# Kernel optimization log

Hardware: AMD Instinct MI355X
Metric: run time of the kernel (lower is better)

## Reference

```python
import jax, jax.numpy as jnp
import numpy as np

HID = 64; H = 2; D = 32; L = 2; G = 64; F_IN = 771
NA = 120000; NE = 60000; E0 = 1500000; E1 = 1000000; E2 = 1000000


def _seg_mean(x, seg, n):
    s = jax.ops.segment_sum(x, seg, num_segments=n)
    c = jax.ops.segment_sum(jnp.ones((x.shape[0], 1), x.dtype), seg, num_segments=n)
    return s / jnp.maximum(c, 1.0)


def setup_inputs() -> dict:
    ks = jax.random.split(jax.random.key(0), 32)
    r = lambda i, s: 0.02 * jax.random.normal(ks[i], s, jnp.float32)
    z = lambda s: jnp.zeros(s, jnp.float32)
    inp = {}
    inp['x_argument'] = jax.random.normal(ks[0], (NA, F_IN), jnp.float32)
    inp['x_evidence'] = jax.random.normal(ks[1], (NE, F_IN), jnp.float32)
    inp['Win'] = r(2, (2, F_IN, HID)); inp['b_in'] = z((2, HID))
    inp['Wk'] = r(3, (L, 2, HID, HID)); inp['bk'] = z((L, 2, HID))
    inp['Wq'] = r(4, (L, 2, HID, HID)); inp['bq'] = z((L, 2, HID))
    inp['Wv'] = r(5, (L, 2, HID, HID)); inp['bv'] = z((L, 2, HID))
    inp['Wa'] = r(6, (L, 2, HID, HID)); inp['ba'] = z((L, 2, HID))
    inp['skip'] = jnp.ones((L, 2), jnp.float32)
    inp['Watt'] = r(7, (L, 3, H, D, D)); inp['Wmsg'] = r(8, (L, 3, H, D, D))
    inp['prel'] = jnp.ones((L, 3, H), jnp.float32)
    inp['Wnews'] = r(9, (384, HID)); inp['bnews'] = z((HID,))
    inp['Wdeb'] = r(10, (HID, HID)); inp['bdeb'] = z((HID,))
    inp['Wqm'] = r(11, (HID, HID)); inp['bqm'] = z((HID,))
    inp['Wkm'] = r(12, (HID, HID)); inp['bkm'] = z((HID,))
    inp['Wvm'] = r(13, (HID, HID)); inp['bvm'] = z((HID,))
    inp['Wom'] = r(14, (HID, HID)); inp['bom'] = z((HID,))
    inp['Wc1'] = r(15, (2 * HID, 64)); inp['bc1'] = z((64,))
    inp['Wc2'] = r(16, (64, 1)); inp['bc2'] = z((1,))
    inp['e0_src'] = jax.random.randint(ks[17], (E0,), 0, NA)
    inp['e0_dst'] = jax.random.randint(ks[18], (E0,), 0, NA)
    inp['e1_src'] = jax.random.randint(ks[19], (E1,), 0, NE)
    inp['e1_dst'] = jax.random.randint(ks[20], (E1,), 0, NA)
    inp['e2_src'] = jax.random.randint(ks[21], (E2,), 0, NA)
    inp['e2_dst'] = jax.random.randint(ks[22], (E2,), 0, NE)
    inp['batch_arg'] = jnp.sort(jax.random.randint(ks[23], (NA,), 0, G))
    return inp


def reference(x_argument, x_evidence, Win, b_in, Wk, bk, Wq, bq, Wv, bv, Wa, ba,
              skip, Watt, Wmsg, prel, Wnews, bnews, Wdeb, bdeb,
              Wqm, bqm, Wkm, bkm, Wvm, bvm, Wom, bom, Wc1, bc1, Wc2, bc2,
              e0_src, e0_dst, e1_src, e1_dst, e2_src, e2_dst, batch_arg):
    # Claim embedding from RAW features (slice 384:768), pooled per graph.
    claim_raw = _seg_mean(x_argument[:, 384:768], batch_arg, G)
    # Per-node-type input projection + ReLU. type 0 = argument, 1 = evidence.
    xs = [jax.nn.relu(x_argument @ Win[0] + b_in[0]),
          jax.nn.relu(x_evidence @ Win[1] + b_in[1])]
    # (src_type, dst_type, src_idx, dst_idx) for each heterogeneous edge type.
    edges = [(0, 0, e0_src, e0_dst), (1, 0, e1_src, e1_dst), (0, 1, e2_src, e2_dst)]
    scale = 1.0 / jnp.sqrt(jnp.float32(D))
    for l in range(L):  # HGTConv stack
        Kt = [(xs[t] @ Wk[l, t] + bk[l, t]).reshape(-1, H, D) for t in range(2)]
        Qt = [(xs[t] @ Wq[l, t] + bq[l, t]).reshape(-1, H, D) for t in range(2)]
        Vt = [(xs[t] @ Wv[l, t] + bv[l, t]).reshape(-1, H, D) for t in range(2)]
        buf = {0: [], 1: []}
        for e, (s, d, src, dst) in enumerate(edges):
            k2 = jnp.einsum('ehd,hdf->ehf', Kt[s][src], Watt[l, e])  # relation key transform
            v2 = jnp.einsum('ehd,hdf->ehf', Vt[s][src], Wmsg[l, e])  # relation msg transform
            sc = (Qt[d][dst] * k2).sum(-1) * prel[l, e] * scale      # (E, H)
            buf[d].append((sc, dst, v2))
        new_xs = []
        for d in range(2):
            n = xs[d].shape[0]
            sc = jnp.concatenate([b[0] for b in buf[d]], 0)
            dst = jnp.concatenate([b[1] for b in buf[d]], 0)
            v2 = jnp.concatenate([b[2] for b in buf[d]], 0)
            # segment softmax over all incoming edges of each destination node
            m = jax.ops.segment_max(sc, dst, num_segments=n)
            ex = jnp.exp(sc - m[dst])
            den = jax.ops.segment_sum(ex, dst, num_segments=n)
            alpha = ex / den[dst]
            agg = jax.ops.segment_sum(alpha[..., None] * v2, dst, num_segments=n).reshape(n, HID)
            out = jax.nn.gelu(agg, approximate=False) @ Wa[l, d] + ba[l, d]
            beta = jax.nn.sigmoid(skip[l, d])
            new_xs.append(beta * out + (1.0 - beta) * xs[d])
        xs = new_xs
    graph_emb = _seg_mean(xs[0], batch_arg, G)
    eF = claim_raw @ Wnews + bnews          # (G, HID)
    g = graph_emb @ Wdeb + bdeb             # (G, HID)
    # MultiheadAttention with query len 1 and key len 1: softmax over a single
    # key is identically 1, so attn_out == out_proj(v_proj(g)) exactly
    # (Wqm/bqm/Wkm/bkm receive exactly zero gradient, matching torch).
    v = g @ Wvm + bvm
    attn_out = v @ Wom + bom
    h = jax.nn.relu(jnp.concatenate([g, attn_out], -1) @ Wc1 + bc1)  # dropout is eval-mode identity
    return h @ Wc2 + bc2  # (G, 1)
```

## Files before the change

kernel.cpp:

```cpp
#include <hip/hip_runtime.h>
#include <math.h>

#define N0 120000
#define N1 60000
#define E0N 1500000
#define E1N 1000000
#define E2N 1000000
#define FIN 771
#define NG 64
#define KSTEPS_IN 25

#define GB0 ((N0 + 127) / 128)
#define GB1 ((N1 + 127) / 128)
#define AB0 ((N0 + 3) / 4)
#define AB1 ((N1 + 3) / 4)
#define SB0 ((N0 + 1023) / 1024)
#define SB1 ((N1 + 1023) / 1024)
#define PREPB 70

#define Q0O   ((size_t)0)
#define KV00O ((size_t)N0 * 64)
#define KV02O ((size_t)N0 * 192)
#define Q1O   ((size_t)N0 * 320)
#define KV11O ((size_t)N0 * 320 + (size_t)N1 * 64)

typedef __attribute__((ext_vector_type(8))) short short8;
typedef __attribute__((ext_vector_type(4))) float f32x4;
typedef __attribute__((ext_vector_type(4))) unsigned short ushort4v;
typedef unsigned short ushort;

__device__ __forceinline__ float gelu_f(float v) {
    return 0.5f * v * (1.f + erff(v * 0.70710678118654752f));
}
__device__ __forceinline__ ushort f2b(float f) {
    union { float f; unsigned u; } v; v.f = f;
    unsigned u = v.u;
    return (ushort)((u + 0x7FFFu + ((u >> 16) & 1u)) >> 16);
}
__device__ __forceinline__ float lo16(unsigned u) {
    union { unsigned x; float f; } v; v.x = u << 16; return v.f;
}
__device__ __forceinline__ float hi16(unsigned u) {
    union { unsigned x; float f; } v; v.x = u & 0xFFFF0000u; return v.f;
}
__device__ __forceinline__ int asi(float f) { union { float f; int i; } v; v.f = f; return v.i; }
__device__ __forceinline__ float asf(int i) { union { int i; float f; } v; v.i = i; return v.f; }

#define GLOAD_LDS16(gsrc, ldst) __builtin_amdgcn_global_load_lds( \
    (const __attribute__((address_space(1))) void*)(gsrc),        \
    (__attribute__((address_space(3))) void*)(ldst), 16, 0, 0)

__device__ __forceinline__ void proj_phase(
    const ushort* xls, int type, int l, int w, int lane, int r0, int nrows,
    const ushort* __restrict__ Wpack, const float* __restrict__ bpack,
    ushort* __restrict__ projAll)
{
    short8 bfr[2][2];
    #pragma unroll
    for (int ksp = 0; ksp < 2; ++ksp)
        #pragma unroll
        for (int rb = 0; rb < 2; ++rb)
            bfr[ksp][rb] = *(const short8*)&xls[(w * 32 + rb * 16 + (lane & 15)) * 72
                                                + ksp * 32 + (lane >> 4) * 8];
    const int nslots = type ? 3 : 5;
    const int sbase = l * 8 + (type ? 5 : 0);
    const int c0b = (lane >> 4) * 4;

    for (int slot = 0; slot < nslots; ++slot) {
        const ushort* Wp = Wpack + (size_t)(sbase + slot) * 4096;
        const float* bias = bpack + (size_t)(sbase + slot) * 64;
        size_t ooff; unsigned pitch, qs, ph;
        if (slot == 0) { ooff = type ? Q1O : Q0O; pitch = 64; qs = 4; ph = 0; }
        else {
            int kv = (slot + 1) >> 1;
            ooff = type ? KV11O : (kv == 1 ? KV00O : KV02O);
            pitch = 128; qs = 8; ph = (slot & 1) ? 0u : 4u;
        }
        ushort* out = projAll + ooff;
        f32x4 acc[2][4] = {};
        #pragma unroll
        for (int ksp = 0; ksp < 2; ++ksp) {
            const ushort* wb = Wp + ksp * 2048 + lane * 8;
            #pragma unroll
            for (int cg = 0; cg < 4; ++cg) {
                short8 afr = *(const short8*)&wb[cg * 512];
                acc[0][cg] = __builtin_amdgcn_mfma_f32_16x16x32_bf16(afr, bfr[ksp][0], acc[0][cg], 0, 0, 0);
                acc[1][cg] = __builtin_amdgcn_mfma_f32_16x16x32_bf16(afr, bfr[ksp][1], acc[1][cg], 0, 0, 0);
            }
        }
        #pragma unroll
        for (int rb = 0; rb < 2; ++rb) {
            int r = r0 + rb * 16 + (lane & 15);
            if (r < nrows) {
                #pragma unroll
                for (int cg = 0; cg < 4; ++cg) {
                    int c = cg * 16 + c0b;
                    ushort4v o;
                    o[0] = f2b(acc[rb][cg][0] + bias[c + 0]);
                    o[1] = f2b(acc[rb][cg][1] + bias[c + 1]);
                    o[2] = f2b(acc[rb][cg][2] + bias[c + 2]);
                    o[3] = f2b(acc[rb][cg][3] + bias[c + 3]);
                    *(ushort4v*)&out[(size_t)r * pitch + (unsigned)(c >> 2) * qs + ph] = o;
                }
            }
        }
    }
}

__global__ __launch_bounds__(256) void inproj_proj_kernel(
    const float* __restrict__ xa, const float* __restrict__ xe,
    const ushort* __restrict__ Wpin, const float* __restrict__ b_in,
    float* __restrict__ xs0, float* __restrict__ xs1,
    const ushort* __restrict__ Wpack, const float* __restrict__ bpack,
    ushort* __restrict__ projAll)
{
    __shared__ union {
        float stage[2][4096];
        ushort xls[128 * 72];
    } sm;
    const int bx = blockIdx.x;
    const int type = (bx >= GB0) ? 1 : 0;
    const float* __restrict__ x = type ? xe : xa;
    const int nrows = type ? N1 : N0;
    const ushort* __restrict__ Wp = Wpin + (type ? (size_t)KSTEPS_IN * 2048 : 0);
    const float* __restrict__ bias = b_in + type * 64;
    float* __restrict__ out = type ? xs1 : xs0;

    const int tid = threadIdx.x, w = tid >> 6, lane = tid & 63;
    const int r0b = (type ? bx - GB0 : bx) * 128;
    const int r0 = r0b + w * 32;
    const float* xlim = x + ((size_t)nrows * FIN - 4);

    const int srow = (lane >> 3);
    const int scol = (lane & 7) * 4;

    f32x4 acc[2][4] = {};

    #pragma unroll
    for (int i = 0; i < 4; ++i) {
        int inst = w * 4 + i;
        int grow = min(r0b + inst * 8 + srow, nrows - 1);
        const float* src = x + (size_t)grow * FIN + scol;
        if (src > xlim) src = xlim;
        GLOAD_LDS16(src, &sm.stage[0][inst * 256]);
    }
    __syncthreads();

    for (int ks = 0; ks < KSTEPS_IN; ++ks) {
        if (ks + 1 < KSTEPS_IN) {
            const int k0 = (ks + 1) * 32;
            float* dbuf = sm.stage[(ks + 1) & 1];
            #pragma unroll
            for (int i = 0; i < 4; ++i) {
                int inst = w * 4 + i;
                int grow = min(r0b + inst * 8 + srow, nrows - 1);
                const float* src = x + (size_t)grow * FIN + k0 + scol;
                if (src > xlim) src = xlim;
                GLOAD_LDS16(src, &dbuf[inst * 256]);
            }
        }
        const float* bufc = sm.stage[ks & 1];
        short8 bfr[2];
        #pragma unroll
        for (int rb = 0; rb < 2; ++rb) {
            int row = w * 32 + rb * 16 + (lane & 15);
            const float* p = bufc + row * 32 + (lane >> 4) * 8;
            float4 f0 = *(const float4*)p;
            float4 f1 = *(const float4*)(p + 4);
            short8 t;
            t[0] = (short)f2b(f0.x); t[1] = (short)f2b(f0.y);
            t[2] = (short)f2b(f0.z); t[3] = (short)f2b(f0.w);
            t[4] = (short)f2b(f1.x); t[5] = (short)f2b(f1.y);
            t[6] = (short)f2b(f1.z); t[7] = (short)f2b(f1.w);
            bfr[rb] = t;
        }
        const ushort* wb = Wp + (size_t)ks * 2048 + lane * 8;
        #pragma unroll
        for (int cg = 0; cg < 4; ++cg) {
            short8 afr = *(const short8*)&wb[cg * 512];
            acc[0][cg] = __builtin_amdgcn_mfma_f32_16x16x32_bf16(afr, bfr[0], acc[0][cg], 0, 0, 0);
            acc[1][cg] = __builtin_amdgcn_mfma_f32_16x16x32_bf16(afr, bfr[1], acc[1][cg], 0, 0, 0);
        }
        __syncthreads();
    }

    const int c0b = (lane >> 4) * 4;
    #pragma unroll
    for (int rb = 0; rb < 2; ++rb) {
        int lrow = w * 32 + rb * 16 + (lane & 15);
        int r = r0b + lrow;
        #pragma unroll
        for (int cg = 0; cg < 4; ++cg) {
            int c = cg * 16 + c0b;
            float4 o;
            o.x = fmaxf(acc[rb][cg][0] + bias[c + 0], 0.f);
            o.y = fmaxf(acc[rb][cg][1] + bias[c + 1], 0.f);
            o.z = fmaxf(acc[rb][cg][2] + bias[c + 2], 0.f);
            o.w = fmaxf(acc[rb][cg][3] + bias[c + 3], 0.f);
            ushort4v h;
            h[0] = f2b(o.x); h[1] = f2b(o.y); h[2] = f2b(o.z); h[3] = f2b(o.w);
            *(ushort4v*)&sm.xls[lrow * 72 + c] = h;
            if (r < nrows) *(float4*)&out[(size_t)r * 64 + c] = o;
        }
    }
    __syncthreads();
    proj_phase(sm.xls, type, 0, w, lane, r0, nrows, Wpack, bpack, projAll);
}

template <int DO_PROJ>
__global__ __launch_bounds__(256) void epi_kernel(
    const float* __restrict__ agg0, const float* __restrict__ agg1,
    const ushort* __restrict__ WaPack, const float* __restrict__ ba,
    float* __restrict__ xs0, float* __restrict__ xs1,
    const float* __restrict__ skip, int l,
    const ushort* __restrict__ Wpack, const float* __restrict__ bpack,
    ushort* __restrict__ projAll)
{
    __shared__ ushort xls[DO_PROJ ? 128 * 72 : 64];
    const int bx = blockIdx.x;
    const int type = (bx >= GB0) ? 1 : 0;
    const float* __restrict__ in = type ? agg1 : agg0;
    float* __restrict__ xs = type ? xs1 : xs0;
    const int nrows = type ? N1 : N0;
    const ushort* __restrict__ Wp = WaPack + (size_t)(l * 2 + type) * 4096;
    const float* __restrict__ bias = ba + (size_t)(l * 2 + type) * 64;
    const float beta = 1.f / (1.f + __expf(-skip[l * 2 + type]));

    const int tid = threadIdx.x, w = tid >> 6, lane = tid & 63;
    const int r0b = (type ? bx - GB0 : bx) * 128;
    const int r0 = r0b + w * 32;
    f32x4 acc[2][4] = {};
    #pragma unroll
    for (int ksp = 0; ksp < 2; ++ksp) {
        short8 bfr[2];
        #pragma unroll
        for (int rb = 0; rb < 2; ++rb) {
            int gr = min(r0 + rb * 16 + (lane & 15), nrows - 1);
            const float* src = in + (size_t)gr * 64 + ksp * 32 + (lane >> 4) * 8;
            float4 f0 = *(const float4*)src;
            float4 f1 = *(const float4*)(src + 4);
            short8 t;
            t[0] = (short)f2b(gelu_f(f0.x)); t[1] = (short)f2b(gelu_f(f0.y));
            t[2] = (short)f2b(gelu_f(f0.z)); t[3] = (short)f2b(gelu_f(f0.w));
            t[4] = (short)f2b(gelu_f(f1.x)); t[5] = (short)f2b(gelu_f(f1.y));
            t[6] = (short)f2b(gelu_f(f1.z)); t[7] = (short)f2b(gelu_f(f1.w));
            bfr[rb] = t;
        }
        const ushort* wb = Wp + ksp * 2048 + lane * 8;
        #pragma unroll
        for (int cg = 0; cg < 4; ++cg) {
            short8 afr = *(const short8*)&wb[cg * 512];
            acc[0][cg] = __builtin_amdgcn_mfma_f32_16x16x32_bf16(afr, bfr[0], acc[0][cg], 0, 0, 0);
            acc[1][cg] = __builtin_amdgcn_mfma_f32_16x16x32_bf16(afr, bfr[1], acc[1][cg], 0, 0, 0);
        }
    }
    const int c0b = (lane >> 4) * 4;
    #pragma unroll
    for (int rb = 0; rb < 2; ++rb) {
        int lrow = w * 32 + rb * 16 + (lane & 15);
        int r = r0b + lrow;
        int gr = min(r, nrows - 1);
        #pragma unroll
        for (int cg = 0; cg < 4; ++cg) {
            int c = cg * 16 + c0b;
            float4 xo = *(const float4*)&xs[(size_t)gr * 64 + c];
            float4 o;
            o.x = beta * (acc[rb][cg][0] + bias[c + 0]) + (1.f - beta) * xo.x;
            o.y = beta * (acc[rb][cg][1] + bias[c + 1]) + (1.f - beta) * xo.y;
            o.z = beta * (acc[rb][cg][2] + bias[c + 2]) + (1.f - beta) * xo.z;
            o.w = beta * (acc[rb][cg][3] + bias[c + 3]) + (1.f - beta) * xo.w;
            if (DO_PROJ) {
                ushort4v h;
                h[0] = f2b(o.x); h[1] = f2b(o.y); h[2] = f2b(o.z); h[3] = f2b(o.w);
                *(ushort4v*)&xls[lrow * 72 + c] = h;
            }
            if (r < nrows) *(float4*)&xs[(size_t)r * 64 + c] = o;
        }
    }
    if (DO_PROJ) {
        __syncthreads();
        proj_phase(xls, type, l + 1, w, lane, r0, nrows, Wpack, bpack, projAll);
    }
}

__global__ __launch_bounds__(256) void prep_zero_kernel(
    const float* __restrict__ Wq, const float* __restrict__ bq,
    const float* __restrict__ Wk, const float* __restrict__ bk,
    const float* __restrict__ Wv, const float* __restrict__ bv,
    const float* __restrict__ Watt, const float* __restrict__ Wmsg,
    const float* __restrict__ prel, const float* __restrict__ Win,
    const float* __restrict__ Wa,
    ushort* __restrict__ Wpack, float* __restrict__ bpack,
    ushort* __restrict__ Wpin, ushort* __restrict__ WaPack,
    int* __restrict__ c0, int* __restrict__ c1,
    int* __restrict__ gs, int* __restrict__ gc)
{
    __shared__ float WF[4096];
    const int b = blockIdx.x;
    const int tid = threadIdx.x;
    if (b >= PREPB) {
        int i = (b - PREPB) * 256 + tid;
        if (i < N0) c0[i] = 0;
        else if (i < N0 + N1) c1[i - N0] = 0;
        else if (i < N0 + N1 + NG * 64) gs[i - N0 - N1] = 0;
        else if (i < N0 + N1 + NG * 64 + NG) gc[i - N0 - N1 - NG * 64] = 0;
        return;
    }
    if (b < 16) {
        const int l = b >> 3;
        const int slot = b & 7;
        const float SCALE = 0.17677669529663689f;
        ushort* outW = Wpack + (size_t)(l * 8 + slot) * 4096;
        float* outB = bpack + (size_t)(l * 8 + slot) * 64;
        const float *Wsrc = 0, *bsrc = 0, *A = 0, *prelE = 0;
        int copy = 0;
        switch (slot) {
            case 0: Wsrc = Wq + (l*2+0)*4096; bsrc = bq + (l*2+0)*64; copy = 1; break;
            case 5: Wsrc = Wq + (l*2+1)*4096; bsrc = bq + (l*2+1)*64; copy = 1; break;
            case 1: Wsrc = Wk + (l*2+0)*4096; bsrc = bk + (l*2+0)*64; A = Watt + (l*3+0)*2048; prelE = prel + l*6 + 0; break;
            case 2: Wsrc = Wv + (l*2+0)*4096; bsrc = bv + (l*2+0)*64; A = Wmsg + (l*3+0)*2048; break;
            case 3: Wsrc = Wk + (l*2+0)*4096; bsrc = bk + (l*2+0)*64; A = Watt + (l*3+2)*2048; prelE = prel + l*6 + 4; break;
            case 4: Wsrc = Wv + (l*2+0)*4096; bsrc = bv + (l*2+0)*64; A = Wmsg + (l*3+2)*2048; break;
            case 6: Wsrc = Wk + (l*2+1)*4096; bsrc = bk + (l*2+1)*64; A = Watt + (l*3+1)*2048; prelE = prel + l*6 + 2; break;
            case 7: Wsrc = Wv + (l*2+1)*4096; bsrc = bv + (l*2+1)*64; A = Wmsg + (l*3+1)*2048; break;
        }
        if (copy) {
            for (int idx = tid; idx < 4096; idx += 256) WF[idx] = Wsrc[idx];
            if (tid < 64) outB[tid] = bsrc[tid];
        } else {
            for (int idx = tid; idx < 4096; idx += 256) {
                int k = idx >> 6, c = idx & 63, h = c >> 5, f = c & 31;
                float s = 0.f;
                for (int d = 0; d < 32; ++d)
                    s += Wsrc[k * 64 + h * 32 + d] * A[(h * 32 + d) * 32 + f];
                if (prelE) s *= prelE[h] * SCALE;
                WF[idx] = s;
            }
            if (tid < 64) {
                int h = tid >> 5, f = tid & 31;
                float s = 0.f;
                for (int d = 0; d < 32; ++d)
                    s += bsrc[h * 32 + d] * A[(h * 32 + d) * 32 + f];
                if (prelE) s *= prelE[h] * SCALE;
                outB[tid] = s;
            }
        }
        __syncthreads();
        for (int idx = tid; idx < 4096; idx += 256) {
            int ksp = idx >> 11, rem = idx & 2047;
            int cg = rem >> 9, rem2 = rem & 511;
            int lane = rem2 >> 3, j = rem2 & 7;
            int k = ksp * 32 + (lane >> 4) * 8 + j;
            int c = cg * 16 + (lane & 15);
            outW[idx] = f2b(WF[k * 64 + c]);
        }
    } else if (b < 16 + 2 * KSTEPS_IN) {
        const int pb = b - 16;
        const int type = pb / KSTEPS_IN, ks = pb % KSTEPS_IN;
        const float* W = Win + (size_t)type * FIN * 64;
        ushort* out = Wpin + (size_t)pb * 2048;
        for (int idx = tid; idx < 2048; idx += 256) {
            int cg = idx >> 9, rem = idx & 511, lane = rem >> 3, j = rem & 7;
            int k = ks * 32 + (lane >> 4) * 8 + j;
            int c = cg * 16 + (lane & 15);
            out[idx] = f2b((k < FIN) ? W[(size_t)k * 64 + c] : 0.f);
        }
    } else {
        const int mb = b - 16 - 2 * KSTEPS_IN;
        const float* W = Wa + (size_t)mb * 4096;
        ushort* o = WaPack + (size_t)mb * 4096;
        for (int idx = tid; idx < 4096; idx += 256) {
            int ksp = idx >> 11, rem = idx & 2047;
            int cg = rem >> 9, rem2 = rem & 511;
            int lane = rem2 >> 3, j = rem2 & 7;
            int k = ksp * 32 + (lane >> 4) * 8 + j;
            int c = cg * 16 + (lane & 15);
            o[idx] = f2b(W[k * 64 + c]);
        }
    }
}

__global__ void hist_all_kernel(
    const int* __restrict__ e0d, const int* __restrict__ e1d, const int* __restrict__ e2d,
    int* __restrict__ cnt0, int* __restrict__ cnt1)
{
    const int total = E0N + E1N + E2N;
    for (int i = blockIdx.x * blockDim.x + threadIdx.x; i < total; i += gridDim.x * blockDim.x) {
        if (i < E0N) atomicAdd(&cnt0[e0d[i]], 1);
        else if (i < E0N + E1N) atomicAdd(&cnt0[e1d[i - E0N]], 1);
        else atomicAdd(&cnt1[e2d[i - E0N - E1N]], 1);
    }
}

__global__ __launch_bounds__(256) void scan1_all_kernel(
    int* __restrict__ cnt0, int* __restrict__ cnt1,
    int* __restrict__ off0, int* __restrict__ off1,
    int* __restrict__ bsA, int* __restrict__ bsB)
{
    __shared__ int sa[256], sb[256];
    const int tid = threadIdx.x;
    const int b = blockIdx.x;
    int* cnt; int n; int* off; int* bsum; int lb;
    if (b < SB0) { cnt = cnt0; n = N0; off = off0; bsum = bsA; lb = b; }
    else { cnt = cnt1; n = N1; off = off1; bsum = bsB; lb = b - SB0; }
    const int base = lb * 1024 + tid * 4;
    int v[4];
    int run = 0;
    #pragma unroll
    for (int i = 0; i < 4; ++i) {
        int x = (base + i < n) ? cnt[base + i] : 0;
        run += x; v[i] = run;
    }
    #pragma unroll
    for (int i = 0; i < 4; ++i)
        if (base + i < n) cnt[base + i] = 0;
    sa[tid] = run;
    __syncthreads();
    int* src = sa; int* dst = sb;
    for (int d = 1; d < 256; d <<= 1) {
        int x = src[tid];
        if (tid >= d) x += src[tid - d];
        dst[tid] = x;
        __syncthreads();
        int* t = src; src = dst; dst = t;
    }
    int excl = src[tid] - run;
    #pragma unroll
    for (int i = 0; i < 4; ++i)
        if (base + i < n) off[base + i + 1] = excl + v[i];
    if (tid == 255) bsum[lb] = src[255];
}

__global__ __launch_bounds__(256) void scan2_all_kernel(int* __restrict__ bsA, int* __restrict__ bsB)
{
    __shared__ int sa[256], sb[256];
    const int tid = threadIdx.x;
    int* bsum = blockIdx.x ? bsB : bsA;
    const int nb = blockIdx.x ? SB1 : SB0;
    int x = (tid < nb) ? bsum[tid] : 0;
    sa[tid] = x;
    __syncthreads();
    int* src = sa; int* dst = sb;
    for (int d = 1; d < 256; d <<= 1) {
        int y = src[tid];
        if (tid >= d) y += src[tid - d];
        dst[tid] = y;
        __syncthreads();
        int* t = src; src = dst; dst = t;
    }
    if (tid < nb) bsum[tid] = src[tid] - x;
}

__global__ __launch_bounds__(256) void scan3_all_kernel(
    int* __restrict__ off0, int* __restrict__ off1,
    const int* __restrict__ bsA, const int* __restrict__ bsB)
{
    const int b = blockIdx.x;
    int* off; const int* boff; int n; int lb;
    if (b < SB0) { off = off0; boff = bsA; n = N0; lb = b; }
    else { off = off1; boff = bsB; n = N1; lb = b - SB0; }
    const int base = lb * 1024 + threadIdx.x * 4;
    const int add = boff[lb];
    #pragma unroll
    for (int i = 0; i < 4; ++i)
        if (base + i < n) off[base + i + 1] += add;
    if (lb == 0 && threadIdx.x == 0) off[0] = 0;
}

__global__ void scatter_all_kernel(
    const int* __restrict__ e0s, const int* __restrict__ e0d,
    const int* __restrict__ e1s, const int* __restrict__ e1d,
    const int* __restrict__ e2s, const int* __restrict__ e2d,
    const int* __restrict__ off0, const int* __restrict__ off1,
    int* __restrict__ cnt0, int* __restrict__ cnt1,
    int* __restrict__ rec0, int* __restrict__ rec1)
{
    const int total = E0N + E1N + E2N;
    for (int i = blockIdx.x * blockDim.x + threadIdx.x; i < total; i += gridDim.x * blockDim.x) {
        if (i < E0N) {
            int d = e0d[i];
            int pos = off0[d] + atomicAdd(&cnt0[d], 1);
            rec0[pos] = e0s[i];
        } else if (i < E0N + E1N) {
            int k = i - E0N;
            int d = e1d[k];
            int pos = off0[d] + atomicAdd(&cnt0[d], 1);
            rec0[pos] = e1s[k] | (1 << 20);
        } else {
            int k = i - E0N - E1N;
            int d = e2d[k];
            int pos = off1[d] + atomicAdd(&cnt1[d], 1);
            rec1[pos] = e2s[k];
        }
    }
}

__global__ __launch_bounds__(256) void agg_fused(
    const int* __restrict__ off0, const int* __restrict__ rec0,
    const int* __restrict__ off1, const int* __restrict__ rec1,
    const ushort* __restrict__ projAll,
    float* __restrict__ agg0, float* __restrict__ agg1)
{
    const int bx = blockIdx.x;
    const int type = (bx >= AB0) ? 1 : 0;
    const int lane = threadIdx.x & 63;
    const int node = (type ? bx - AB0 : bx) * 4 + (threadIdx.x >> 6);
    const int ndst = type ? N1 : N0;
    if (node >= ndst) return;
    const int* __restrict__ off = type ? off1 : off0;
    const int* __restrict__ rec = type ? rec1 : rec0;
    const ushort* __restrict__ Q   = projAll + (type ? Q1O : Q0O);
    const ushort* __restrict__ KVa = projAll + (type ? KV02O : KV00O);
    const ushort* __restrict__ KVb = projAll + (type ? KV02O : KV11O);
    float* __restrict__ outAgg = type ? agg1 : agg0;

    const int grp = lane >> 4;
    const int gi  = lane & 15;
    float q0, q1, q2, q3;
    {
        const unsigned* qp = (const unsigned*)(Q + (size_t)node * 64 + gi * 4);
        unsigned u0 = qp[0], u1 = qp[1];
        q0 = lo16(u0); q1 = hi16(u0); q2 = lo16(u1); q3 = hi16(u1);
    }
    const int s = off[node], e = off[node + 1];
    float den = 0.f, a0 = 0.f, a1 = 0.f, a2 = 0.f, a3 = 0.f;
    for (int j = s; j < e; j += 16) {
        bool v[4]; uint4 kv[4]; float p[4];
        #pragma unroll
        for (int q = 0; q < 4; ++q) {
            int jj = j + grp + q * 4;
            v[q] = jj < e;
            int r = rec[v[q] ? jj : s];
            const ushort* KV = (r & (1 << 20)) ? KVb : KVa;
            kv[q] = *(const uint4*)(KV + ((size_t)(unsigned)(r & 0xFFFFF) << 7) + gi * 8);
        }
        #pragma unroll
        for (int q = 0; q < 4; ++q)
            p[q] = lo16(kv[q].x) * q0 + hi16(kv[q].x) * q1 + lo16(kv[q].y) * q2 + hi16(kv[q].y) * q3;
        #pragma unroll
        for (int q = 0; q < 4; ++q) p[q] += asf(__builtin_amdgcn_ds_swizzle(asi(p[q]), 0x041F));
        #pragma unroll
        for (int q = 0; q < 4; ++q) p[q] += asf(__builtin_amdgcn_ds_swizzle(asi(p[q]), 0x081F));
        #pragma unroll
        for (int q = 0; q < 4; ++q) p[q] += asf(__builtin_amdgcn_ds_swizzle(asi(p[q]), 0x101F));
        #pragma unroll
        for (int q = 0; q < 4; ++q) {
            float wgt = v[q] ? __expf(p[q]) : 0.f;
            den += wgt;
            a0 = fmaf(wgt, lo16(kv[q].z), a0);
            a1 = fmaf(wgt, hi16(kv[q].z), a1);
            a2 = fmaf(wgt, lo16(kv[q].w), a2);
            a3 = fmaf(wgt, hi16(kv[q].w), a3);
        }
    }
    a0 += __shfl_xor(a0, 16); a0 += __shfl_xor(a0, 32);
    a1 += __shfl_xor(a1, 16); a1 += __shfl_xor(a1, 32);
    a2 += __shfl_xor(a2, 16); a2 += __shfl_xor(a2, 32);
    a3 += __shfl_xor(a3, 16); a3 += __shfl_xor(a3, 32);
    den += __shfl_xor(den, 16); den += __shfl_xor(den, 32);
    if (lane < 16) {
        float inv = (den > 0.f) ? 1.f / den : 0.f;
        float4 o;
        o.x = a0 * inv; o.y = a1 * inv; o.z = a2 * inv; o.w = a3 * inv;
        *(float4*)&outAgg[(size_t)node * 64 + gi * 4] = o;
    }
}

__global__ __launch_bounds__(256) void segsum_kernel(
    const float* __restrict__ xs, const int* __restrict__ seg, int n,
    float* __restrict__ gsum, int* __restrict__ gcnt)
{
    const int lane = threadIdx.x & 63;
    const int wid = blockIdx.x * 4 + (threadIdx.x >> 6);
    const int rbeg = wid * 256;
    if (rbeg >= n) return;
    const int rend = min(rbeg + 256, n);
    float s = 0.f;
    int cur = seg[rbeg];
    int run = 0;
    for (int r = rbeg; r < rend; ++r) {
        int sg = seg[r];
        if (sg != cur) {
            atomicAdd(&gsum[cur * 64 + lane], s);
            if (lane == 0) atomicAdd(&gcnt[cur], run);
            cur = sg; s = 0.f; run = 0;
        }
        s += xs[(size_t)r * 64 + lane];
        run++;
    }
    atomicAdd(&gsum[cur * 64 + lane], s);
    if (lane == 0) atomicAdd(&gcnt[cur], run);
}

__global__ __launch_bounds__(256) void head_kernel(
    const float* __restrict__ gsum, const int* __restrict__ gcnt,
    const float* __restrict__ Wdeb, const float* __restrict__ bdeb,
    const float* __restrict__ Wvm, const float* __restrict__ bvm,
    const float* __restrict__ Wom, const float* __restrict__ bom,
    const float* __restrict__ Wc1, const float* __restrict__ bc1,
    const float* __restrict__ Wc2, const float* __restrict__ bc2,
    float* __restrict__ outp)
{
    __shared__ float A[4096], B[4096], C[4096];
    const int tid = threadIdx.x;
    for (int idx = tid; idx < 4096; idx += 256) {
        int g = idx >> 6;
        A[idx] = gsum[idx] / fmaxf((float)gcnt[g], 1.f);
    }
    __syncthreads();
    for (int idx = tid; idx < 4096; idx += 256) {
        int g = idx >> 6, c = idx & 63;
        float s = bdeb[c];
        for (int k = 0; k < 64; ++k) s = fmaf(A[g * 64 + k], Wdeb[k * 64 + c], s);
        B[idx] = s;
    }
    __syncthreads();
    for (int idx = tid; idx < 4096; idx += 256) {
        int g = idx >> 6, c = idx & 63;
        float s = bvm[c];
        for (int k = 0; k < 64; ++k) s = fmaf(B[g * 64 + k], Wvm[k * 64 + c], s);
        C[idx] = s;
    }
    __syncthreads();
    for (int idx = tid; idx < 4096; idx += 256) {
        int g = idx >> 6, c = idx & 63;
        float s = bom[c];
        for (int k = 0; k < 64; ++k) s = fmaf(C[g * 64 + k], Wom[k * 64 + c], s);
        A[idx] = s;
    }
    __syncthreads();
    for (int idx = tid; idx < 4096; idx += 256) {
        int g = idx >> 6, c = idx & 63;
        float s = bc1[c];
        for (int k = 0; k < 64; ++k) s = fmaf(B[g * 64 + k], Wc1[k * 64 + c], s);
        for (int k = 0; k < 64; ++k) s = fmaf(A[g * 64 + k], Wc1[(64 + k) * 64 + c], s);
        C[idx] = fmaxf(s, 0.f);
    }
    __syncthreads();
    if (tid < 64) {
        float s = bc2[0];
        for (int c = 0; c < 64; ++c) s = fmaf(C[tid * 64 + c], Wc2[c], s);
        outp[tid] = s;
    }
}

extern "C" void kernel_launch(void* const* d_in, const int* in_sizes, int n_in,
                              void* d_out, int out_size, void* d_ws, size_t ws_size,
                              hipStream_t stream)
{
    const float* x_arg = (const float*)d_in[0];
    const float* x_ev  = (const float*)d_in[1];
    const float* Win   = (const float*)d_in[2];
    const float* b_in  = (const float*)d_in[3];
    const float* Wk    = (const float*)d_in[4];
    const float* bk    = (const float*)d_in[5];
    const float* Wq    = (const float*)d_in[6];
    const float* bq    = (const float*)d_in[7];
    const float* Wv    = (const float*)d_in[8];
    const float* bv    = (const float*)d_in[9];
    const float* Wa    = (const float*)d_in[10];
    const float* ba    = (const float*)d_in[11];
    const float* skip  = (const float*)d_in[12];
    const float* Watt  = (const float*)d_in[13];
    const float* Wmsg  = (const float*)d_in[14];
    const float* prel  = (const float*)d_in[15];
    const float* Wdeb  = (const float*)d_in[18];
    const float* bdeb  = (const float*)d_in[19];
    const float* Wvm   = (const float*)d_in[24];
    const float* bvm   = (const float*)d_in[25];
    const float* Wom   = (const float*)d_in[26];
    const float* bom   = (const float*)d_in[27];
    const float* Wc1   = (const float*)d_in[28];
    const float* bc1   = (const float*)d_in[29];
    const float* Wc2   = (const float*)d_in[30];
    const float* bc2   = (const float*)d_in[31];
    const int* e0s = (const int*)d_in[32];
    const int* e0d = (const int*)d_in[33];
    const int* e1s = (const int*)d_in[34];
    const int* e1d = (const int*)d_in[35];
    const int* e2s = (const int*)d_in[36];
    const int* e2d = (const int*)d_in[37];
    const int* batch = (const int*)d_in[38];
    float* outp = (float*)d_out;

    char* w = (char*)d_ws;
    size_t o = 0;
    auto alloc = [&](size_t bytes) -> char* {
        char* p = w + o;
        o = (o + bytes + 255) & ~(size_t)255;
        return p;
    };
    float* xs0   = (float*)alloc((size_t)N0 * 64 * 4);
    float* xs1   = (float*)alloc((size_t)N1 * 64 * 4);
    ushort* projAll = (ushort*)alloc(((size_t)N0 * 320 + (size_t)N1 * 192) * 2);
    float* agg0  = (float*)alloc((size_t)N0 * 64 * 4);
    float* agg1  = (float*)alloc((size_t)N1 * 64 * 4);
    int* off0 = (int*)alloc((size_t)(N0 + 1) * 4);
    int* off1 = (int*)alloc((size_t)(N1 + 1) * 4);
    int* cnt0 = (int*)alloc((size_t)N0 * 4);
    int* cnt1 = (int*)alloc((size_t)N1 * 4);
    int* rec0 = (int*)alloc((size_t)(E0N + E1N) * 4);
    int* rec1 = (int*)alloc((size_t)E2N * 4);
    int* bsA  = (int*)alloc(256 * 4);
    int* bsB  = (int*)alloc(256 * 4);
    ushort* Wpack = (ushort*)alloc((size_t)16 * 4096 * 2);
    float* bpack = (float*)alloc((size_t)16 * 64 * 4);
    ushort* Wpin = (ushort*)alloc((size_t)2 * KSTEPS_IN * 2048 * 2);
    ushort* WaPack = (ushort*)alloc((size_t)4 * 4096 * 2);
    float* gsum = (float*)alloc((size_t)NG * 64 * 4);
    int* gcnt = (int*)alloc((size_t)NG * 4);
    if (o > ws_size) return;

    const int ZB = (N0 + N1 + NG * 64 + NG + 255) / 256;

    prep_zero_kernel<<<PREPB + ZB, 256, 0, stream>>>(
        Wq, bq, Wk, bk, Wv, bv, Watt, Wmsg, prel, Win, Wa,
        Wpack, bpack, Wpin, WaPack, cnt0, cnt1, (int*)gsum, gcnt);
    hist_all_kernel<<<1280, 256, 0, stream>>>(e0d, e1d, e2d, cnt0, cnt1);
    scan1_all_kernel<<<SB0 + SB1, 256, 0, stream>>>(cnt0, cnt1, off0, off1, bsA, bsB);
    scan2_all_kernel<<<2, 256, 0, stream>>>(bsA, bsB);
    scan3_all_kernel<<<SB0 + SB1, 256, 0, stream>>>(off0, off1, bsA, bsB);
    scatter_all_kernel<<<1280, 256, 0, stream>>>(
        e0s, e0d, e1s, e1d, e2s, e2d, off0, off1, cnt0, cnt1, rec0, rec1);
    inproj_proj_kernel<<<GB0 + GB1, 256, 0, stream>>>(
        x_arg, x_ev, Wpin, b_in, xs0, xs1, Wpack, bpack, projAll);
    agg_fused<<<AB0 + AB1, 256, 0, stream>>>(off0, rec0, off1, rec1, projAll, agg0, agg1);
    epi_kernel<1><<<GB0 + GB1, 256, 0, stream>>>(
        agg0, agg1, WaPack, ba, xs0, xs1, skip, 0, Wpack, bpack, projAll);
    agg_fused<<<AB0 + AB1, 256, 0, stream>>>(off0, rec0, off1, rec1, projAll, agg0, agg1);
    epi_kernel<0><<<GB0 + GB1, 256, 0, stream>>>(
        agg0, agg1, WaPack, ba, xs0, xs1, skip, 1, Wpack, bpack, projAll);
    {
        int waves = (N0 + 255) / 256;
        segsum_kernel<<<(waves + 3) / 4, 256, 0, stream>>>(xs0, batch, N0, gsum, gcnt);
    }
    head_kernel<<<1, 256, 0, stream>>>(gsum, gcnt, Wdeb, bdeb, Wvm, bvm, Wom, bom,
                                       Wc1, bc1, Wc2, bc2, outp);
}
```

Measured before the change: 1.064 ms.

## Stage projection outputs through LDS and load input in large swizzled chunks

The projection phase now writes each group's bf16 outputs into an LDS scratch tile and then copies whole 128-row blocks to global memory with coalesced 16-byte stores, instead of scattered 8-byte stores. The input projection GEMM replaces its 32-column double-buffered staging with 128-column chunks loaded into LDS using an XOR swizzle to avoid bank conflicts. The 3-column tail is handled with direct global loads. The aim is fewer, wider memory transactions. In exchange it drops the overlap between loading and compute, adds barriers, and uses much more LDS (64KB per block), which may lower occupancy.

```diff
diff --git a/kernel.cpp b/kernel.cpp
--- a/kernel.cpp
+++ b/kernel.cpp
@@ -51,7 +51,8 @@
     (__attribute__((address_space(3))) void*)(ldst), 16, 0, 0)
 
 __device__ __forceinline__ void proj_phase(
-    const ushort* xls, int type, int l, int w, int lane, int r0, int nrows,
+    const ushort* xls, ushort* scratch, int type, int l, int w, int lane, int tid,
+    int r0b, int nrows,
     const ushort* __restrict__ Wpack, const float* __restrict__ bpack,
     ushort* __restrict__ projAll)
 {
@@ -62,36 +63,34 @@
         for (int rb = 0; rb < 2; ++rb)
             bfr[ksp][rb] = *(const short8*)&xls[(w * 32 + rb * 16 + (lane & 15)) * 72
                                                 + ksp * 32 + (lane >> 4) * 8];
-    const int nslots = type ? 3 : 5;
     const int sbase = l * 8 + (type ? 5 : 0);
     const int c0b = (lane >> 4) * 4;
-
-    for (int slot = 0; slot < nslots; ++slot) {
-        const ushort* Wp = Wpack + (size_t)(sbase + slot) * 4096;
-        const float* bias = bpack + (size_t)(sbase + slot) * 64;
-        size_t ooff; unsigned pitch, qs, ph;
-        if (slot == 0) { ooff = type ? Q1O : Q0O; pitch = 64; qs = 4; ph = 0; }
-        else {
-            int kv = (slot + 1) >> 1;
-            ooff = type ? KV11O : (kv == 1 ? KV00O : KV02O);
-            pitch = 128; qs = 8; ph = (slot & 1) ? 0u : 4u;
-        }
-        ushort* out = projAll + ooff;
-        f32x4 acc[2][4] = {};
-        #pragma unroll
-        for (int ksp = 0; ksp < 2; ++ksp) {
-            const ushort* wb = Wp + ksp * 2048 + lane * 8;
+    const int ngroups = type ? 2 : 3;
+
+    for (int grp = 0; grp < ngroups; ++grp) {
+        const int s0 = (grp == 0) ? 0 : (grp * 2 - 1);
+        const int nsl = (grp == 0) ? 1 : 2;
+        const unsigned pitch = (grp == 0) ? 64u : 128u;
+        const unsigned qs = (grp == 0) ? 4u : 8u;
+        for (int si = 0; si < nsl; ++si) {
+            const int slot = s0 + si;
+            const ushort* Wp = Wpack + (size_t)(sbase + slot) * 4096;
+            const float* bias = bpack + (size_t)(sbase + slot) * 64;
+            const unsigned ph = (grp == 0) ? 0u : (si ? 4u : 0u);
+            f32x4 acc[2][4] = {};
             #pragma unroll
-            for (int cg = 0; cg < 4; ++cg) {
-                short8 afr = *(const short8*)&wb[cg * 512];
-                acc[0][cg] = __builtin_amdgcn_mfma_f32_16x16x32_bf16(afr, bfr[ksp][0], acc[0][cg], 0, 0, 0);
-                acc[1][cg] = __builtin_amdgcn_mfma_f32_16x16x32_bf16(afr, bfr[ksp][1], acc[1][cg], 0, 0, 0);
+            for (int ksp = 0; ksp < 2; ++ksp) {
+                const ushort* wb = Wp + ksp * 2048 + lane * 8;
+                #pragma unroll
+                for (int cg = 0; cg < 4; ++cg) {
+                    short8 afr = *(const short8*)&wb[cg * 512];
+                    acc[0][cg] = __builtin_amdgcn_mfma_f32_16x16x32_bf16(afr, bfr[ksp][0], acc[0][cg], 0, 0, 0);
+                    acc[1][cg] = __builtin_amdgcn_mfma_f32_16x16x32_bf16(afr, bfr[ksp][1], acc[1][cg], 0, 0, 0);
+                }
             }
-        }
-        #pragma unroll
-        for (int rb = 0; rb < 2; ++rb) {
-            int r = r0 + rb * 16 + (lane & 15);
-            if (r < nrows) {
+            #pragma unroll
+            for (int rb = 0; rb < 2; ++rb) {
+                int lrow = w * 32 + rb * 16 + (lane & 15);
                 #pragma unroll
                 for (int cg = 0; cg < 4; ++cg) {
                     int c = cg * 16 + c0b;
@@ -100,10 +99,25 @@
                     o[1] = f2b(acc[rb][cg][1] + bias[c + 1]);
                     o[2] = f2b(acc[rb][cg][2] + bias[c + 2]);
                     o[3] = f2b(acc[rb][cg][3] + bias[c + 3]);
-                    *(ushort4v*)&out[(size_t)r * pitch + (unsigned)(c >> 2) * qs + ph] = o;
+                    *(ushort4v*)&scratch[(unsigned)lrow * pitch + (unsigned)(c >> 2) * qs + ph] = o;
                 }
             }
         }
+        __syncthreads();
+        size_t ooff;
+        if (grp == 0) ooff = type ? Q1O : Q0O;
+        else if (grp == 1) ooff = type ? KV11O : KV00O;
+        else ooff = KV02O;
+        char* outg = (char*)(projAll + ooff + (size_t)r0b * pitch);
+        const int rowBytes = (int)pitch * 2;
+        const int totalBytes = 128 * rowBytes;
+        for (int q = 0; q < totalBytes / 4096; ++q) {
+            int off = q * 4096 + tid * 16;
+            int row = off / rowBytes;
+            if (r0b + row < nrows)
+                *(uint4*)(outg + off) = *(const uint4*)((const char*)scratch + off);
+        }
+        __syncthreads();
     }
 }
 
@@ -115,8 +129,8 @@
     ushort* __restrict__ projAll)
 {
     __shared__ union {
-        float stage[2][4096];
-        ushort xls[128 * 72];
+        float stage[128 * 128];
+        struct { ushort xls[128 * 72]; ushort scratch[128 * 128]; } pp;
     } sm;
     const int bx = blockIdx.x;
     const int type = (bx >= GB0) ? 1 : 0;
@@ -128,62 +142,64 @@
 
     const int tid = threadIdx.x, w = tid >> 6, lane = tid & 63;
     const int r0b = (type ? bx - GB0 : bx) * 128;
-    const int r0 = r0b + w * 32;
-    const float* xlim = x + ((size_t)nrows * FIN - 4);
-
-    const int srow = (lane >> 3);
-    const int scol = (lane & 7) * 4;
 
     f32x4 acc[2][4] = {};
 
-    #pragma unroll
-    for (int i = 0; i < 4; ++i) {
-        int inst = w * 4 + i;
-        int grow = min(r0b + inst * 8 + srow, nrows - 1);
-        const float* src = x + (size_t)grow * FIN + scol;
-        if (src > xlim) src = xlim;
-        GLOAD_LDS16(src, &sm.stage[0][inst * 256]);
-    }
-    __syncthreads();
-
-    for (int ks = 0; ks < KSTEPS_IN; ++ks) {
-        if (ks + 1 < KSTEPS_IN) {
-            const int k0 = (ks + 1) * 32;
-            float* dbuf = sm.stage[(ks + 1) & 1];
+    for (int m = 0; m < 6; ++m) {
+        const int k0 = m * 128;
+        #pragma unroll
+        for (int i = 0; i < 16; ++i) {
+            int inst = w * 16 + i;
+            int grow = min(r0b + inst * 2 + (lane >> 5), nrows - 1);
+            int col = ((((lane & 31) >> 1) ^ (grow & 15)) << 3) | ((lane & 1) << 2);
+            GLOAD_LDS16(x + (size_t)grow * FIN + k0 + col, &sm.stage[inst * 256]);
+        }
+        __syncthreads();
+        #pragma unroll
+        for (int ks = 0; ks < 4; ++ks) {
+            short8 bfr[2];
             #pragma unroll
-            for (int i = 0; i < 4; ++i) {
-                int inst = w * 4 + i;
-                int grow = min(r0b + inst * 8 + srow, nrows - 1);
-                const float* src = x + (size_t)grow * FIN + k0 + scol;
-                if (src > xlim) src = xlim;
-                GLOAD_LDS16(src, &dbuf[inst * 256]);
+            for (int rb = 0; rb < 2; ++rb) {
+                int row = w * 32 + rb * 16 + (lane & 15);
+                int slot = (ks * 4 + (lane >> 4)) ^ (row & 15);
+                const float* p = &sm.stage[row * 128 + slot * 8];
+                float4 f0 = *(const float4*)p;
+                float4 f1 = *(const float4*)(p + 4);
+                short8 t;
+                t[0] = (short)f2b(f0.x); t[1] = (short)f2b(f0.y);
+                t[2] = (short)f2b(f0.z); t[3] = (short)f2b(f0.w);
+                t[4] = (short)f2b(f1.x); t[5] = (short)f2b(f1.y);
+                t[6] = (short)f2b(f1.z); t[7] = (short)f2b(f1.w);
+                bfr[rb] = t;
             }
-        }
-        const float* bufc = sm.stage[ks & 1];
-        short8 bfr[2];
-        #pragma unroll
-        for (int rb = 0; rb < 2; ++rb) {
-            int row = w * 32 + rb * 16 + (lane & 15);
-            const float* p = bufc + row * 32 + (lane >> 4) * 8;
-            float4 f0 = *(const float4*)p;
-            float4 f1 = *(const float4*)(p + 4);
-            short8 t;
-            t[0] = (short)f2b(f0.x); t[1] = (short)f2b(f0.y);
-            t[2] = (short)f2b(f0.z); t[3] = (short)f2b(f0.w);
-            t[4] = (short)f2b(f1.x); t[5] = (short)f2b(f1.y);
-            t[6] = (short)f2b(f1.z); t[7] = (short)f2b(f1.w);
-            bfr[rb] = t;
-        }
-        const ushort* wb = Wp + (size_t)ks * 2048 + lane * 8;
+            const ushort* wb = Wp + (size_t)(m * 4 + ks) * 2048 + lane * 8;
+            #pragma unroll
+            for (int cg = 0; cg < 4; ++cg) {
+                short8 afr = *(const short8*)&wb[cg * 512];
+                acc[0][cg] = __builtin_amdgcn_mfma_f32_16x16x32_bf16(afr, bfr[0], acc[0][cg], 0, 0, 0);
+                acc[1][cg] = __builtin_amdgcn_mfma_f32_16x16x32_bf16(afr, bfr[1], acc[1][cg], 0, 0, 0);
+            }
+        }
+        __syncthreads();
+    }
+    {
+        const int rA = min(r0b + w * 32 + (lane & 15), nrows - 1);
+        const int rB = min(r0b + w * 32 + 16 + (lane & 15), nrows - 1);
+        short8 bA = {}, bB = {};
+        if ((lane >> 4) == 0) {
+            const float* tA = x + (size_t)rA * FIN + 768;
+            const float* tB = x + (size_t)rB * FIN + 768;
+            bA[0] = (short)f2b(tA[0]); bA[1] = (short)f2b(tA[1]); bA[2] = (short)f2b(tA[2]);
+            bB[0] = (short)f2b(tB[0]); bB[1] = (short)f2b(tB[1]); bB[2] = (short)f2b(tB[2]);
+        }
+        const ushort* wb = Wp + (size_t)24 * 2048 + lane * 8;
         #pragma unroll
         for (int cg = 0; cg < 4; ++cg) {
             short8 afr = *(const short8*)&wb[cg * 512];
-            acc[0][cg] = __builtin_amdgcn_mfma_f32_16x16x32_bf16(afr, bfr[0], acc[0][cg], 0, 0, 0);
-            acc[1][cg] = __builtin_amdgcn_mfma_f32_16x16x32_bf16(afr, bfr[1], acc[1][cg], 0, 0, 0);
-        }
-        __syncthreads();
-    }
-
+            acc[0][cg] = __builtin_amdgcn_mfma_f32_16x16x32_bf16(afr, bA, acc[0][cg], 0, 0, 0);
+            acc[1][cg] = __builtin_amdgcn_mfma_f32_16x16x32_bf16(afr, bB, acc[1][cg], 0, 0, 0);
+        }
+    }
     const int c0b = (lane >> 4) * 4;
     #pragma unroll
     for (int rb = 0; rb < 2; ++rb) {
@@ -199,12 +215,12 @@
             o.w = fmaxf(acc[rb][cg][3] + bias[c + 3], 0.f);
             ushort4v h;
             h[0] = f2b(o.x); h[1] = f2b(o.y); h[2] = f2b(o.z); h[3] = f2b(o.w);
-            *(ushort4v*)&sm.xls[lrow * 72 + c] = h;
+            *(ushort4v*)&sm.pp.xls[lrow * 72 + c] = h;
             if (r < nrows) *(float4*)&out[(size_t)r * 64 + c] = o;
         }
     }
     __syncthreads();
-    proj_phase(sm.xls, type, 0, w, lane, r0, nrows, Wpack, bpack, projAll);
+    proj_phase(sm.pp.xls, sm.pp.scratch, type, 0, w, lane, tid, r0b, nrows, Wpack, bpack, projAll);
 }
 
 template <int DO_PROJ>
@@ -217,6 +233,7 @@
     ushort* __restrict__ projAll)
 {
     __shared__ ushort xls[DO_PROJ ? 128 * 72 : 64];
+    __shared__ ushort scratch[DO_PROJ ? 128 * 128 : 64];
     const int bx = blockIdx.x;
     const int type = (bx >= GB0) ? 1 : 0;
     const float* __restrict__ in = type ? agg1 : agg0;
@@ -279,7 +296,7 @@
     }
     if (DO_PROJ) {
         __syncthreads();
-        proj_phase(xls, type, l + 1, w, lane, r0, nrows, Wpack, bpack, projAll);
+        proj_phase(xls, scratch, type, l + 1, w, lane, tid, r0b, nrows, Wpack, bpack, projAll);
     }
 }
 
```

After: 1.078 ms. No clear change (+1.3%).
